# Performance work log

Hardware: AMD Instinct MI355X
Metric: run time of the kernel (lower is better)

The kernel has to match this reference:

```python
import jax, jax.numpy as jnp
import numpy as np

DE_NEIGHBORS = 3
DEPTH = 2


def square_distance(src, dst):
    # src: [B, N, 3], dst: [B, S, 3] -> pairwise squared L2 [B, N, S]
    return (jnp.sum(src * src, axis=-1)[:, :, None]
            + jnp.sum(dst * dst, axis=-1)[:, None, :]
            - 2.0 * jnp.einsum('bnc,bsc->bns', src, dst))


def propagate(xyz1, xyz2, points1, points2):
    # xyz1: [B, N, 3] fine coords; xyz2: [B, S, 3] coarse coords
    # points1: [B, C1, N] skip feats; points2: [B, C2, S] coarse feats
    pts2 = points2.transpose(0, 2, 1)  # [B, S, C2]
    dists = square_distance(xyz1, xyz2)  # [B, N, S]
    neg_d, idx = jax.lax.top_k(-dists, DE_NEIGHBORS)  # smallest-k distances
    d = -neg_d  # [B, N, K]
    w = 1.0 / (d + 1e-8)
    w = w / jnp.sum(w, axis=-1, keepdims=True)  # [B, N, K]
    # gather neighbor features: [B, N, K, C2]
    gathered = jax.vmap(lambda p, i: p[i])(pts2, idx)
    interp = jnp.sum(gathered * w[..., None], axis=2)  # [B, N, C2]
    m = interp.mean()
    s = jnp.std(interp - m, ddof=1)  # torch.std default is unbiased
    interp = (interp - m) / (s + 1e-5)
    new_points = jnp.concatenate([points1.transpose(0, 2, 1), interp], axis=-1)
    return new_points.transpose(0, 2, 1)  # [B, C1+C2, N]


def setup_inputs() -> dict:
    key = jax.random.key(0)
    ks = jax.random.split(key, 6)
    B = 8
    return {
        'xyz0': jax.random.normal(ks[0], (B, 8192, 3), jnp.float32),
        'xyz1': jax.random.normal(ks[1], (B, 2048, 3), jnp.float32),
        'xyz2': jax.random.normal(ks[2], (B, 512, 3), jnp.float32),
        'x0': jax.random.normal(ks[3], (B, 128, 8192), jnp.float32),
        'x1': jax.random.normal(ks[4], (B, 256, 2048), jnp.float32),
        'x2': jax.random.normal(ks[5], (B, 512, 512), jnp.float32),
    }


def reference(xyz0, xyz1, xyz2, x0, x1, x2):
    # forward reverses the lists: index 0 = coarsest level
    xyz_list = [xyz2, xyz1, xyz0]
    x_list = [x2, x1, x0]
    x = x_list[0]
    for i in range(DEPTH):
        x = propagate(xyz_list[i + 1], xyz_list[i], x_list[i + 1], x)
    return x  # [8, 128+256+512, 8192]
```

## Files before the change

kernel.cpp:

```cpp
#include <hip/hip_runtime.h>
#include <cstdint>
#include <math.h>


__device__ __forceinline__ void dev_transpose(const float* __restrict__ in,
                                              float* __restrict__ out,
                                              int C, long in_bs, long out_bs, int out_rs,
                                              int b, int rt, int ct, int tid) {
    __shared__ float tile[32][33];
    const int r0 = rt * 32, c0 = ct * 32;
    const float* inb = in + (size_t)b * in_bs;
    float* outb = out + (size_t)b * out_bs;
    const int tx = tid & 31, ty = tid >> 5;
#pragma unroll
    for (int i = 0; i < 32; i += 8) {
        tile[ty + i][tx] = inb[(size_t)(r0 + ty + i) * C + (c0 + tx)];
    }
    __syncthreads();
#pragma unroll
    for (int i = 0; i < 32; i += 8) {
        outb[(size_t)(c0 + ty + i) * out_rs + (r0 + tx)] = tile[tx][ty + i];
    }
}

__global__ __launch_bounds__(256) void k_setup(const float* __restrict__ xyz1,
                                               const float* __restrict__ xyz2,
                                               const float* __restrict__ x0,
                                               const float* __restrict__ x1,
                                               const float* __restrict__ x2,
                                               float4* __restrict__ c4_2,
                                               float4* __restrict__ c4_1,
                                               float* __restrict__ pts1,
                                               float* __restrict__ inter,
                                               float* __restrict__ out) {
#pragma clang fp contract(off)
    const int id = blockIdx.x;
    const int tid = threadIdx.x;
    if (id < 8192) {
        const size_t i = (size_t)id * 256 + tid;
        const size_t b = i >> 18;
        const size_t off = i & (((size_t)1 << 18) - 1);
        const float4* src = (const float4*)(x0 + b * (size_t)128 * 8192);
        float4* dst = (float4*)(out + b * (size_t)896 * 8192);
        dst[off] = src[off];
    } else if (id < 12288) {
        const int t = id - 8192;
        const int ct = t & 63, rt = (t >> 6) & 7, b = t >> 9;
        dev_transpose(x1, inter, 2048, 256 * 2048, (long)2048 * 768, 768, b, rt, ct, tid);
    } else if (id < 14336) {
        const int t = id - 12288;
        const int ct = t & 15, rt = (t >> 4) & 15, b = t >> 8;
        dev_transpose(x2, pts1, 512, 512 * 512, 512 * 512, 512, b, rt, ct, tid);
    } else {
        const int i = (id - 14336) * 256 + tid;
        const float* src;
        float4* dst;
        if (i < 16384) { src = xyz1 + 3 * (size_t)i; dst = c4_2 + i; }
        else if (i < 20480) { src = xyz2 + 3 * (size_t)(i - 16384); dst = c4_1 + (i - 16384); }
        else return;
        const float x = src[0], y = src[1], z = src[2];
        *dst = make_float4(x, y, z, (x * x + y * y) + z * z);
    }
}

template <int CHUNK>
__device__ __forceinline__ void dev_knn_scan(const float* __restrict__ fine,
                                             const float4* __restrict__ coarse4,
                                             int N, int S, int nch,
                                             int b, int nb, int chunk, int tid,
                                             float* __restrict__ cand_d,
                                             int* __restrict__ cand_i) {
#pragma clang fp contract(off)
    const int n = nb * 256 + tid;
    const int s0 = chunk * CHUNK;
    const float4* cb = coarse4 + (size_t)b * S + s0;
    const float* fp = fine + ((size_t)b * N + n) * 3;
    const float px = fp[0], py = fp[1], pz = fp[2];
    const float psq = (px * px + py * py) + pz * pz;
    float d0 = 1e30f, d1 = 1e30f, d2 = 1e30f;
    int i0 = 0, i1 = 0, i2 = 0;
#pragma unroll 4
    for (int s = 0; s < CHUNK; ++s) {
        const float4 c = cb[s];
        const float dot = (px * c.x + py * c.y) + pz * c.z;
        const float d = fmaf(-2.0f, dot, psq + c.w);
        if (__any(d < d2)) {
            const bool lt0 = d < d0, lt1 = d < d1, lt2 = d < d2;
            d2 = lt1 ? d1 : (lt2 ? d : d2);
            i2 = lt1 ? i1 : (lt2 ? s : i2);
            d1 = lt0 ? d0 : (lt1 ? d : d1);
            i1 = lt0 ? i0 : (lt1 ? s : i1);
            d0 = lt0 ? d : d0;
            i0 = lt0 ? s : i0;
        }
    }
    const size_t p = (((size_t)b * N + n) * nch + chunk) * 3;
    cand_d[p] = d0; cand_d[p + 1] = d1; cand_d[p + 2] = d2;
    cand_i[p] = s0 + i0; cand_i[p + 1] = s0 + i1; cand_i[p + 2] = s0 + i2;
}

__global__ __launch_bounds__(256) void k_knn_all(const float* __restrict__ xyz0,
                                                 const float4* __restrict__ c4_2,
                                                 const float* __restrict__ xyz1,
                                                 const float4* __restrict__ c4_1,
                                                 float* __restrict__ cand_d2,
                                                 int* __restrict__ cand_i2,
                                                 float* __restrict__ cand_d1,
                                                 int* __restrict__ cand_i1) {
    const int id = blockIdx.x;
    const int tid = threadIdx.x;
    if (id < 1024) {
        dev_knn_scan<512>(xyz0, c4_2, 8192, 2048, 4,
                          id >> 7, id & 31, (id >> 5) & 3, tid, cand_d2, cand_i2);
    } else {
        const int t = id - 1024;
        dev_knn_scan<128>(xyz1, c4_1, 2048, 512, 4,
                          t >> 5, t & 7, (t >> 3) & 3, tid, cand_d1, cand_i1);
    }
}

__global__ __launch_bounds__(256) void k_merge(const float* __restrict__ cand_d2,
                                               const int* __restrict__ cand_i2,
                                               const float* __restrict__ cand_d1,
                                               const int* __restrict__ cand_i1,
                                               int* __restrict__ idx2,
                                               float* __restrict__ w2,
                                               int* __restrict__ idx1,
                                               float* __restrict__ w1) {
    int p = blockIdx.x * 256 + threadIdx.x;
    const float* cd; const int* ci; int* idx; float* wout;
    if (p < 65536) { cd = cand_d2; ci = cand_i2; idx = idx2; wout = w2; }
    else { p -= 65536; cd = cand_d1; ci = cand_i1; idx = idx1; wout = w1; }
    cd += (size_t)p * 12; ci += (size_t)p * 12;
    float d0 = 1e30f, d1 = 1e30f, d2 = 1e30f;
    int i0 = 0, i1 = 0, i2 = 0;
#pragma unroll
    for (int k = 0; k < 12; ++k) {
        const float d = cd[k];
        const int s = ci[k];
        const bool lt0 = d < d0, lt1 = d < d1, lt2 = d < d2;
        d2 = lt1 ? d1 : (lt2 ? d : d2);
        i2 = lt1 ? i1 : (lt2 ? s : i2);
        d1 = lt0 ? d0 : (lt1 ? d : d1);
        i1 = lt0 ? i0 : (lt1 ? s : i1);
        d0 = lt0 ? d : d0;
        i0 = lt0 ? s : i0;
    }
    const float w0 = 1.0f / (d0 + 1e-8f);
    const float w1_ = 1.0f / (d1 + 1e-8f);
    const float w2_ = 1.0f / (d2 + 1e-8f);
    const float wsum = (w0 + w1_) + w2_;
    const size_t q = (size_t)p * 3;
    idx[q] = i0; idx[q + 1] = i1; idx[q + 2] = i2;
    wout[q] = w0 / wsum; wout[q + 1] = w1_ / wsum; wout[q + 2] = w2_ / wsum;
}

__global__ __launch_bounds__(256) void k_interp_stats(const float* __restrict__ pts,
                                                      const int* __restrict__ idx,
                                                      const float* __restrict__ w,
                                                      int N, int S, int C,
                                                      double* __restrict__ partials) {
    __shared__ int   si[32][3];
    __shared__ float sw[32][3];
    const int b = blockIdx.x, nb = blockIdx.y, cb = blockIdx.z;
    const int n0 = nb * 32;
    const int tid = threadIdx.x;
    if (tid < 32) {
        size_t p = ((size_t)b * N + n0 + tid) * 3;
        si[tid][0] = idx[p]; si[tid][1] = idx[p + 1]; si[tid][2] = idx[p + 2];
        sw[tid][0] = w[p];   sw[tid][1] = w[p + 1];   sw[tid][2] = w[p + 2];
    }
    __syncthreads();
    const int C4 = C >> 2;
    const float4* pbf = (const float4*)(pts + (size_t)b * S * C) + (cb * 64);
    const int f = tid & 63;
    const int pg = tid >> 6;
    double ls = 0.0, lq = 0.0;
#pragma unroll
    for (int g = 0; g < 8; ++g) {
        const int nl = g * 4 + pg;
        const size_t r0 = (size_t)si[nl][0] * C4;
        const size_t r1 = (size_t)si[nl][1] * C4;
        const size_t r2 = (size_t)si[nl][2] * C4;
        const float w0 = sw[nl][0], w1 = sw[nl][1], w2 = sw[nl][2];
        const float4 a = pbf[r0 + f], c = pbf[r1 + f], e = pbf[r2 + f];
        const float vx = (w0 * a.x + w1 * c.x) + w2 * e.x;
        const float vy = (w0 * a.y + w1 * c.y) + w2 * e.y;
        const float vz = (w0 * a.z + w1 * c.z) + w2 * e.z;
        const float vw = (w0 * a.w + w1 * c.w) + w2 * e.w;
        ls += (double)vx + (double)vy + (double)vz + (double)vw;
        lq += (double)vx * vx + (double)vy * vy + (double)vz * vz + (double)vw * vw;
    }
    __shared__ double sa[256], sb[256];
    sa[tid] = ls; sb[tid] = lq; __syncthreads();
    for (int s = 128; s > 0; s >>= 1) {
        if (tid < s) { sa[tid] += sa[tid + s]; sb[tid] += sb[tid + s]; }
        __syncthreads();
    }
    if (tid == 0) {
        size_t pl = ((size_t)cb * gridDim.x + b) * gridDim.y + nb;
        partials[2 * pl] = sa[0]; partials[2 * pl + 1] = sb[0];
    }
}

__global__ __launch_bounds__(1024) void k_finalize(const double* __restrict__ partials,
                                                   int P, double nelem,
                                                   float* __restrict__ stats) {
    __shared__ double sa[1024], sb[1024];
    double ls = 0.0, lq = 0.0;
    for (int i = threadIdx.x; i < P; i += 1024) { ls += partials[2 * i]; lq += partials[2 * i + 1]; }
    const int t = threadIdx.x;
    sa[t] = ls; sb[t] = lq; __syncthreads();
    for (int s = 512; s > 0; s >>= 1) {
        if (t < s) { sa[t] += sa[t + s]; sb[t] += sb[t + s]; }
        __syncthreads();
    }
    if (t == 0) {
        double sum = sa[0], sq = sb[0];
        double m = sum / nelem;
        double var = (sq - sum * sum / nelem) / (nelem - 1.0);
        double sd = sqrt(var > 0.0 ? var : 0.0);
        stats[0] = (float)m;
        stats[1] = (float)(1.0 / (sd + 1e-5));
    }
}

__global__ __launch_bounds__(256) void k_interp1_write(const float* __restrict__ pts,
                                                       const int* __restrict__ idx,
                                                       const float* __restrict__ w,
                                                       const float* __restrict__ stats,
                                                       float* __restrict__ inter) {
    const float m = stats[0], rs = stats[1];
    const int b = blockIdx.x;
    const int n0 = blockIdx.y * 4;
    const int tid = threadIdx.x;
    const int pt = tid >> 6, f = tid & 63;
    const size_t p = (size_t)b * 2048 + n0 + pt;
    const int i0 = idx[p * 3], i1 = idx[p * 3 + 1], i2 = idx[p * 3 + 2];
    const float w0 = w[p * 3], w1 = w[p * 3 + 1], w2 = w[p * 3 + 2];
    const float4* pb4 = (const float4*)(pts + (size_t)b * 512 * 512);
    const size_t r0 = (size_t)i0 * 128, r1 = (size_t)i1 * 128, r2 = (size_t)i2 * 128;
    float4* out4 = (float4*)(inter + p * 768 + 256);
#pragma unroll
    for (int k = 0; k < 2; ++k) {
        const int c = f + k * 64;
        const float4 a = pb4[r0 + c], d = pb4[r1 + c], e = pb4[r2 + c];
        float4 v;
        v.x = (((w0 * a.x + w1 * d.x) + w2 * e.x) - m) * rs;
        v.y = (((w0 * a.y + w1 * d.y) + w2 * e.y) - m) * rs;
        v.z = (((w0 * a.z + w1 * d.z) + w2 * e.z) - m) * rs;
        v.w = (((w0 * a.w + w1 * d.w) + w2 * e.w) - m) * rs;
        out4[c] = v;
    }
}

__global__ __launch_bounds__(256) void k_interp2_write(const float* __restrict__ pts,
                                                       const int* __restrict__ idx,
                                                       const float* __restrict__ w,
                                                       const float* __restrict__ stats,
                                                       float* __restrict__ out) {
    __shared__ float tile[64][65];
    __shared__ int   si[64][3];
    __shared__ float sw[64][3];
    const float m = stats[0], rs = stats[1];
    const int b = blockIdx.x, nt = blockIdx.y, cc = blockIdx.z;
    const int n0 = nt * 64, c0 = cc * 64;
    const int tid = threadIdx.x;
    if (tid < 64) {
        size_t p = ((size_t)b * 8192 + n0 + tid) * 3;
        si[tid][0] = idx[p]; si[tid][1] = idx[p + 1]; si[tid][2] = idx[p + 2];
        sw[tid][0] = w[p];   sw[tid][1] = w[p + 1];   sw[tid][2] = w[p + 2];
    }
    __syncthreads();
    const float* pb = pts + (size_t)b * 2048 * 768 + c0;
    const int cl = tid & 63;
    const int pg = tid >> 6;
#pragma unroll
    for (int pass = 0; pass < 16; ++pass) {
        const int nl = pass * 4 + pg;
        const float v = (sw[nl][0] * pb[(size_t)si[nl][0] * 768 + cl]
                       + sw[nl][1] * pb[(size_t)si[nl][1] * 768 + cl])
                       + sw[nl][2] * pb[(size_t)si[nl][2] * 768 + cl];
        tile[nl][cl] = (v - m) * rs;
    }
    __syncthreads();
    float* ob = out + (size_t)b * 896 * 8192 + (size_t)(128 + c0) * 8192 + n0;
    const int tn = tid & 63, tc0 = tid >> 6;
#pragma unroll
    for (int pass = 0; pass < 16; ++pass) {
        const int tc = pass * 4 + tc0;
        ob[(size_t)tc * 8192 + tn] = tile[tn][tc];
    }
}

extern "C" void kernel_launch(void* const* d_in, const int* in_sizes, int n_in,
                              void* d_out, int out_size, void* d_ws, size_t ws_size,
                              hipStream_t stream) {
    const float* xyz0 = (const float*)d_in[0];
    const float* xyz1 = (const float*)d_in[1];
    const float* xyz2 = (const float*)d_in[2];
    const float* x0   = (const float*)d_in[3];
    const float* x1   = (const float*)d_in[4];
    const float* x2   = (const float*)d_in[5];
    float* out = (float*)d_out;
    char* ws = (char*)d_ws;

    size_t off = 0;
    auto alloc = [&](size_t bytes) {
        size_t o = off;
        off = (off + bytes + 255) & ~(size_t)255;
        return o;
    };
    float*  stats    = (float*)(ws + alloc(4 * sizeof(float)));
    double* partials = (double*)(ws + alloc((size_t)6144 * 2 * sizeof(double)));
    int*    idx1     = (int*)(ws + alloc((size_t)8 * 2048 * 3 * 4));
    float*  w1       = (float*)(ws + alloc((size_t)8 * 2048 * 3 * 4));
    int*    idx2     = (int*)(ws + alloc((size_t)8 * 8192 * 3 * 4));
    float*  w2       = (float*)(ws + alloc((size_t)8 * 8192 * 3 * 4));
    float4* c4_2     = (float4*)(ws + alloc((size_t)16384 * 16));
    float4* c4_1     = (float4*)(ws + alloc((size_t)4096 * 16));
    float*  pts1     = (float*)(ws + alloc((size_t)8 * 512 * 512 * 4));
    float*  inter    = (float*)(ws + alloc((size_t)8 * 2048 * 768 * 4));
    float*  cand_d2  = (float*)(ws + alloc((size_t)65536 * 12 * 4));
    int*    cand_i2  = (int*)(ws + alloc((size_t)65536 * 12 * 4));
    float*  cand_d1  = (float*)(ws + alloc((size_t)16384 * 12 * 4));
    int*    cand_i1  = (int*)(ws + alloc((size_t)16384 * 12 * 4));

    k_setup<<<14416, 256, 0, stream>>>(xyz1, xyz2, x0, x1, x2,
                                       c4_2, c4_1, pts1, inter, out);
    k_knn_all<<<1280, 256, 0, stream>>>(xyz0, c4_2, xyz1, c4_1,
                                        cand_d2, cand_i2, cand_d1, cand_i1);
    k_merge<<<(65536 + 16384) / 256, 256, 0, stream>>>(cand_d2, cand_i2, cand_d1, cand_i1,
                                                       idx2, w2, idx1, w1);
    k_interp_stats<<<dim3(8, 2048 / 32, 2), 256, 0, stream>>>(
        pts1, idx1, w1, 2048, 512, 512, partials);
    k_finalize<<<1, 1024, 0, stream>>>(partials, 1024, (double)8 * 2048 * 512, stats);
    k_interp1_write<<<dim3(8, 512), 256, 0, stream>>>(pts1, idx1, w1, stats, inter);
    k_interp_stats<<<dim3(8, 8192 / 32, 3), 256, 0, stream>>>(
        inter, idx2, w2, 8192, 2048, 768, partials);
    k_finalize<<<1, 1024, 0, stream>>>(partials, 6144, (double)8 * 8192 * 768, stats + 2);
    k_interp2_write<<<dim3(8, 128, 12), 256, 0, stream>>>(inter, idx2, w2, stats + 2, out);
}
```

Before: 198.5 us.

## Fuse setup and KNN into one front kernel, fold merge and finalize into consumers

```diff
diff --git a/kernel.cpp b/kernel.cpp
--- a/kernel.cpp
+++ b/kernel.cpp
@@ -3,77 +3,49 @@
 #include <math.h>
 
 
-__device__ __forceinline__ void dev_transpose(const float* __restrict__ in,
-                                              float* __restrict__ out,
-                                              int C, long in_bs, long out_bs, int out_rs,
-                                              int b, int rt, int ct, int tid) {
-    __shared__ float tile[32][33];
-    const int r0 = rt * 32, c0 = ct * 32;
-    const float* inb = in + (size_t)b * in_bs;
-    float* outb = out + (size_t)b * out_bs;
-    const int tx = tid & 31, ty = tid >> 5;
-#pragma unroll
-    for (int i = 0; i < 32; i += 8) {
-        tile[ty + i][tx] = inb[(size_t)(r0 + ty + i) * C + (c0 + tx)];
-    }
-    __syncthreads();
-#pragma unroll
-    for (int i = 0; i < 32; i += 8) {
-        outb[(size_t)(c0 + ty + i) * out_rs + (r0 + tx)] = tile[tx][ty + i];
-    }
-}
-
-__global__ __launch_bounds__(256) void k_setup(const float* __restrict__ xyz1,
-                                               const float* __restrict__ xyz2,
-                                               const float* __restrict__ x0,
-                                               const float* __restrict__ x1,
-                                               const float* __restrict__ x2,
-                                               float4* __restrict__ c4_2,
-                                               float4* __restrict__ c4_1,
-                                               float* __restrict__ pts1,
-                                               float* __restrict__ inter,
-                                               float* __restrict__ out) {
+__device__ __forceinline__ void dev_merge6(const float* __restrict__ cd,
+                                           const int* __restrict__ ci,
+                                           int& o0, int& o1, int& o2,
+                                           float& w0, float& w1, float& w2) {
+    float d0 = 1e30f, d1 = 1e30f, d2 = 1e30f;
+    int j0 = 0, j1 = 0, j2 = 0;
+#pragma unroll
+    for (int k = 0; k < 6; ++k) {
+        const float d = cd[k];
+        const int s = ci[k];
+        const bool lt0 = d < d0, lt1 = d < d1, lt2 = d < d2;
+        d2 = lt1 ? d1 : (lt2 ? d : d2);
+        j2 = lt1 ? j1 : (lt2 ? s : j2);
+        d1 = lt0 ? d0 : (lt1 ? d : d1);
+        j1 = lt0 ? j0 : (lt1 ? s : j1);
+        d0 = lt0 ? d : d0;
+        j0 = lt0 ? s : j0;
+    }
+    const float a = 1.0f / (d0 + 1e-8f);
+    const float b = 1.0f / (d1 + 1e-8f);
+    const float c = 1.0f / (d2 + 1e-8f);
+    const float ws = (a + b) + c;
+    o0 = j0; o1 = j1; o2 = j2;
+    w0 = a / ws; w1 = b / ws; w2 = c / ws;
+}
+
+template <int CHUNK>
+__device__ __forceinline__ void dev_knn_lds(const float* __restrict__ fine,
+                                            const float* __restrict__ coarse,
+                                            int N, int S, int nch,
+                                            int b, int nb, int chunk, int tid,
+                                            float4* __restrict__ lc,
+                                            float* __restrict__ cand_d,
+                                            int* __restrict__ cand_i) {
 #pragma clang fp contract(off)
-    const int id = blockIdx.x;
-    const int tid = threadIdx.x;
-    if (id < 8192) {
-        const size_t i = (size_t)id * 256 + tid;
-        const size_t b = i >> 18;
-        const size_t off = i & (((size_t)1 << 18) - 1);
-        const float4* src = (const float4*)(x0 + b * (size_t)128 * 8192);
-        float4* dst = (float4*)(out + b * (size_t)896 * 8192);
-        dst[off] = src[off];
-    } else if (id < 12288) {
-        const int t = id - 8192;
-        const int ct = t & 63, rt = (t >> 6) & 7, b = t >> 9;
-        dev_transpose(x1, inter, 2048, 256 * 2048, (long)2048 * 768, 768, b, rt, ct, tid);
-    } else if (id < 14336) {
-        const int t = id - 12288;
-        const int ct = t & 15, rt = (t >> 4) & 15, b = t >> 8;
-        dev_transpose(x2, pts1, 512, 512 * 512, 512 * 512, 512, b, rt, ct, tid);
-    } else {
-        const int i = (id - 14336) * 256 + tid;
-        const float* src;
-        float4* dst;
-        if (i < 16384) { src = xyz1 + 3 * (size_t)i; dst = c4_2 + i; }
-        else if (i < 20480) { src = xyz2 + 3 * (size_t)(i - 16384); dst = c4_1 + (i - 16384); }
-        else return;
-        const float x = src[0], y = src[1], z = src[2];
-        *dst = make_float4(x, y, z, (x * x + y * y) + z * z);
-    }
-}
-
-template <int CHUNK>
-__device__ __forceinline__ void dev_knn_scan(const float* __restrict__ fine,
-                                             const float4* __restrict__ coarse4,
-                                             int N, int S, int nch,
-                                             int b, int nb, int chunk, int tid,
-                                             float* __restrict__ cand_d,
-                                             int* __restrict__ cand_i) {
-#pragma clang fp contract(off)
+    const int s0 = chunk * CHUNK;
+    const float* cb = coarse + ((size_t)b * S + s0) * 3;
+    for (int s = tid; s < CHUNK; s += 256) {
+        const float x = cb[3 * s], y = cb[3 * s + 1], z = cb[3 * s + 2];
+        lc[s] = make_float4(x, y, z, (x * x + y * y) + z * z);
+    }
+    __syncthreads();
     const int n = nb * 256 + tid;
-    const int s0 = chunk * CHUNK;
-    const float4* cb = coarse4 + (size_t)b * S + s0;
     const float* fp = fine + ((size_t)b * N + n) * 3;
     const float px = fp[0], py = fp[1], pz = fp[2];
     const float psq = (px * px + py * py) + pz * pz;
@@ -81,7 +53,7 @@
     int i0 = 0, i1 = 0, i2 = 0;
 #pragma unroll 4
     for (int s = 0; s < CHUNK; ++s) {
-        const float4 c = cb[s];
+        const float4 c = lc[s];
         const float dot = (px * c.x + py * c.y) + pz * c.z;
         const float d = fmaf(-2.0f, dot, psq + c.w);
         if (__any(d < d2)) {
@@ -99,76 +71,91 @@
     cand_i[p] = s0 + i0; cand_i[p + 1] = s0 + i1; cand_i[p + 2] = s0 + i2;
 }
 
-__global__ __launch_bounds__(256) void k_knn_all(const float* __restrict__ xyz0,
-                                                 const float4* __restrict__ c4_2,
-                                                 const float* __restrict__ xyz1,
-                                                 const float4* __restrict__ c4_1,
-                                                 float* __restrict__ cand_d2,
-                                                 int* __restrict__ cand_i2,
-                                                 float* __restrict__ cand_d1,
-                                                 int* __restrict__ cand_i1) {
+__device__ __forceinline__ void dev_transpose(const float* __restrict__ in,
+                                              float* __restrict__ out,
+                                              int C, long in_bs, long out_bs, int out_rs,
+                                              int b, int rt, int ct, int tid,
+                                              float* __restrict__ tile ) {
+    const int r0 = rt * 32, c0 = ct * 32;
+    const float* inb = in + (size_t)b * in_bs;
+    float* outb = out + (size_t)b * out_bs;
+    const int tx = tid & 31, ty = tid >> 5;
+#pragma unroll
+    for (int i = 0; i < 32; i += 8) {
+        tile[(ty + i) * 33 + tx] = inb[(size_t)(r0 + ty + i) * C + (c0 + tx)];
+    }
+    __syncthreads();
+#pragma unroll
+    for (int i = 0; i < 32; i += 8) {
+        outb[(size_t)(c0 + ty + i) * out_rs + (r0 + tx)] = tile[tx * 33 + (ty + i)];
+    }
+}
+
+__global__ __launch_bounds__(256) void k_front(const float* __restrict__ xyz0,
+                                               const float* __restrict__ xyz1,
+                                               const float* __restrict__ xyz2,
+                                               const float* __restrict__ x0,
+                                               const float* __restrict__ x1,
+                                               const float* __restrict__ x2,
+                                               float* __restrict__ pts1,
+                                               float* __restrict__ inter,
+                                               float* __restrict__ out,
+                                               float* __restrict__ cand_d2,
+                                               int* __restrict__ cand_i2,
+                                               float* __restrict__ cand_d1,
+                                               int* __restrict__ cand_i1,
+                                               unsigned* __restrict__ counters) {
+    __shared__ __align__(16) char smem[16384];
     const int id = blockIdx.x;
     const int tid = threadIdx.x;
-    if (id < 1024) {
-        dev_knn_scan<512>(xyz0, c4_2, 8192, 2048, 4,
-                          id >> 7, id & 31, (id >> 5) & 3, tid, cand_d2, cand_i2);
+    if (id < 512) {
+        dev_knn_lds<1024>(xyz0, xyz1, 8192, 2048, 2,
+                          id >> 6, id & 31, (id >> 5) & 1, tid,
+                          (float4*)smem, cand_d2, cand_i2);
+    } else if (id < 640) {
+        const int t = id - 512;
+        dev_knn_lds<256>(xyz1, xyz2, 2048, 512, 2,
+                         t >> 4, t & 7, (t >> 3) & 1, tid,
+                         (float4*)smem, cand_d1, cand_i1);
+    } else if (id < 8832) {
+        if (id == 640 && tid < 2) counters[tid] = 0;
+        const size_t i = (size_t)(id - 640) * 256 + tid;
+        const size_t b = i >> 18;
+        const size_t off = i & (((size_t)1 << 18) - 1);
+        const float4* src = (const float4*)(x0 + b * (size_t)128 * 8192);
+        float4* dst = (float4*)(out + b * (size_t)896 * 8192);
+        dst[off] = src[off];
+    } else if (id < 12928) {
+        const int t = id - 8832;
+        const int ct = t & 63, rt = (t >> 6) & 7, b = t >> 9;
+        dev_transpose(x1, inter, 2048, 256 * 2048, (long)2048 * 768, 768,
+                      b, rt, ct, tid, (float*)smem);
     } else {
-        const int t = id - 1024;
-        dev_knn_scan<128>(xyz1, c4_1, 2048, 512, 4,
-                          t >> 5, t & 7, (t >> 3) & 3, tid, cand_d1, cand_i1);
-    }
-}
-
-__global__ __launch_bounds__(256) void k_merge(const float* __restrict__ cand_d2,
-                                               const int* __restrict__ cand_i2,
-                                               const float* __restrict__ cand_d1,
-                                               const int* __restrict__ cand_i1,
-                                               int* __restrict__ idx2,
-                                               float* __restrict__ w2,
-                                               int* __restrict__ idx1,
-                                               float* __restrict__ w1) {
-    int p = blockIdx.x * 256 + threadIdx.x;
-    const float* cd; const int* ci; int* idx; float* wout;
-    if (p < 65536) { cd = cand_d2; ci = cand_i2; idx = idx2; wout = w2; }
-    else { p -= 65536; cd = cand_d1; ci = cand_i1; idx = idx1; wout = w1; }
-    cd += (size_t)p * 12; ci += (size_t)p * 12;
-    float d0 = 1e30f, d1 = 1e30f, d2 = 1e30f;
-    int i0 = 0, i1 = 0, i2 = 0;
-#pragma unroll
-    for (int k = 0; k < 12; ++k) {
-        const float d = cd[k];
-        const int s = ci[k];
-        const bool lt0 = d < d0, lt1 = d < d1, lt2 = d < d2;
-        d2 = lt1 ? d1 : (lt2 ? d : d2);
-        i2 = lt1 ? i1 : (lt2 ? s : i2);
-        d1 = lt0 ? d0 : (lt1 ? d : d1);
-        i1 = lt0 ? i0 : (lt1 ? s : i1);
-        d0 = lt0 ? d : d0;
-        i0 = lt0 ? s : i0;
-    }
-    const float w0 = 1.0f / (d0 + 1e-8f);
-    const float w1_ = 1.0f / (d1 + 1e-8f);
-    const float w2_ = 1.0f / (d2 + 1e-8f);
-    const float wsum = (w0 + w1_) + w2_;
-    const size_t q = (size_t)p * 3;
-    idx[q] = i0; idx[q + 1] = i1; idx[q + 2] = i2;
-    wout[q] = w0 / wsum; wout[q + 1] = w1_ / wsum; wout[q + 2] = w2_ / wsum;
+        const int t = id - 12928;
+        const int ct = t & 15, rt = (t >> 4) & 15, b = t >> 8;
+        dev_transpose(x2, pts1, 512, 512 * 512, 512 * 512, 512,
+                      b, rt, ct, tid, (float*)smem);
+    }
 }
 
 __global__ __launch_bounds__(256) void k_interp_stats(const float* __restrict__ pts,
-                                                      const int* __restrict__ idx,
-                                                      const float* __restrict__ w,
+                                                      const float* __restrict__ cand_d,
+                                                      const int* __restrict__ cand_i,
                                                       int N, int S, int C,
-                                                      double* __restrict__ partials) {
+                                                      double* __restrict__ partials,
+                                                      float* __restrict__ stats_out,
+                                                      unsigned* __restrict__ counter,
+                                                      int nblocks, double nelem) {
     __shared__ int   si[32][3];
     __shared__ float sw[32][3];
     const int b = blockIdx.x, nb = blockIdx.y, cb = blockIdx.z;
     const int n0 = nb * 32;
     const int tid = threadIdx.x;
     if (tid < 32) {
-        size_t p = ((size_t)b * N + n0 + tid) * 3;
-        si[tid][0] = idx[p]; si[tid][1] = idx[p + 1]; si[tid][2] = idx[p + 2];
-        sw[tid][0] = w[p];   sw[tid][1] = w[p + 1];   sw[tid][2] = w[p + 2];
+        const size_t pt = (size_t)b * N + n0 + tid;
+        dev_merge6(cand_d + pt * 6, cand_i + pt * 6,
+                   si[tid][0], si[tid][1], si[tid][2],
+                   sw[tid][0], sw[tid][1], sw[tid][2]);
     }
     __syncthreads();
     const int C4 = C >> 2;
@@ -197,37 +184,38 @@
         if (tid < s) { sa[tid] += sa[tid + s]; sb[tid] += sb[tid + s]; }
         __syncthreads();
     }
+    __shared__ unsigned ticket;
     if (tid == 0) {
-        size_t pl = ((size_t)cb * gridDim.x + b) * gridDim.y + nb;
+        const size_t pl = ((size_t)cb * gridDim.x + b) * gridDim.y + nb;
         partials[2 * pl] = sa[0]; partials[2 * pl + 1] = sb[0];
-    }
-}
-
-__global__ __launch_bounds__(1024) void k_finalize(const double* __restrict__ partials,
-                                                   int P, double nelem,
-                                                   float* __restrict__ stats) {
-    __shared__ double sa[1024], sb[1024];
-    double ls = 0.0, lq = 0.0;
-    for (int i = threadIdx.x; i < P; i += 1024) { ls += partials[2 * i]; lq += partials[2 * i + 1]; }
-    const int t = threadIdx.x;
-    sa[t] = ls; sb[t] = lq; __syncthreads();
-    for (int s = 512; s > 0; s >>= 1) {
-        if (t < s) { sa[t] += sa[t + s]; sb[t] += sb[t + s]; }
-        __syncthreads();
-    }
-    if (t == 0) {
-        double sum = sa[0], sq = sb[0];
-        double m = sum / nelem;
-        double var = (sq - sum * sum / nelem) / (nelem - 1.0);
-        double sd = sqrt(var > 0.0 ? var : 0.0);
-        stats[0] = (float)m;
-        stats[1] = (float)(1.0 / (sd + 1e-5));
+        __threadfence();
+        ticket = atomicAdd(counter, 1u);
+    }
+    __syncthreads();
+    if (ticket == (unsigned)(nblocks - 1)) {
+        __threadfence();
+        double fs = 0.0, fq = 0.0;
+        for (int i = tid; i < nblocks; i += 256) { fs += partials[2 * i]; fq += partials[2 * i + 1]; }
+        sa[tid] = fs; sb[tid] = fq; __syncthreads();
+        for (int s = 128; s > 0; s >>= 1) {
+            if (tid < s) { sa[tid] += sa[tid + s]; sb[tid] += sb[tid + s]; }
+            __syncthreads();
+        }
+        if (tid == 0) {
+            const double sum = sa[0], sq = sb[0];
+            const double m = sum / nelem;
+            const double var = (sq - sum * sum / nelem) / (nelem - 1.0);
+            const double sd = sqrt(var > 0.0 ? var : 0.0);
+            stats_out[0] = (float)m;
+            stats_out[1] = (float)(1.0 / (sd + 1e-5));
+            *counter = 0;
+        }
     }
 }
 
 __global__ __launch_bounds__(256) void k_interp1_write(const float* __restrict__ pts,
-                                                       const int* __restrict__ idx,
-                                                       const float* __restrict__ w,
+                                                       const float* __restrict__ cand_d,
+                                                       const int* __restrict__ cand_i,
                                                        const float* __restrict__ stats,
                                                        float* __restrict__ inter) {
     const float m = stats[0], rs = stats[1];
@@ -236,8 +224,8 @@
     const int tid = threadIdx.x;
     const int pt = tid >> 6, f = tid & 63;
     const size_t p = (size_t)b * 2048 + n0 + pt;
-    const int i0 = idx[p * 3], i1 = idx[p * 3 + 1], i2 = idx[p * 3 + 2];
-    const float w0 = w[p * 3], w1 = w[p * 3 + 1], w2 = w[p * 3 + 2];
+    int i0, i1, i2; float w0, w1, w2;
+    dev_merge6(cand_d + p * 6, cand_i + p * 6, i0, i1, i2, w0, w1, w2);
     const float4* pb4 = (const float4*)(pts + (size_t)b * 512 * 512);
     const size_t r0 = (size_t)i0 * 128, r1 = (size_t)i1 * 128, r2 = (size_t)i2 * 128;
     float4* out4 = (float4*)(inter + p * 768 + 256);
@@ -255,8 +243,8 @@
 }
 
 __global__ __launch_bounds__(256) void k_interp2_write(const float* __restrict__ pts,
-                                                       const int* __restrict__ idx,
-                                                       const float* __restrict__ w,
+                                                       const float* __restrict__ cand_d,
+                                                       const int* __restrict__ cand_i,
                                                        const float* __restrict__ stats,
                                                        float* __restrict__ out) {
     __shared__ float tile[64][65];
@@ -267,9 +255,10 @@
     const int n0 = nt * 64, c0 = cc * 64;
     const int tid = threadIdx.x;
     if (tid < 64) {
-        size_t p = ((size_t)b * 8192 + n0 + tid) * 3;
-        si[tid][0] = idx[p]; si[tid][1] = idx[p + 1]; si[tid][2] = idx[p + 2];
-        sw[tid][0] = w[p];   sw[tid][1] = w[p + 1];   sw[tid][2] = w[p + 2];
+        const size_t pt = (size_t)b * 8192 + n0 + tid;
+        dev_merge6(cand_d + pt * 6, cand_i + pt * 6,
+                   si[tid][0], si[tid][1], si[tid][2],
+                   sw[tid][0], sw[tid][1], sw[tid][2]);
     }
     __syncthreads();
     const float* pb = pts + (size_t)b * 2048 * 768 + c0;
@@ -311,33 +300,26 @@
         off = (off + bytes + 255) & ~(size_t)255;
         return o;
     };
-    float*  stats    = (float*)(ws + alloc(4 * sizeof(float)));
-    double* partials = (double*)(ws + alloc((size_t)6144 * 2 * sizeof(double)));
-    int*    idx1     = (int*)(ws + alloc((size_t)8 * 2048 * 3 * 4));
-    float*  w1       = (float*)(ws + alloc((size_t)8 * 2048 * 3 * 4));
-    int*    idx2     = (int*)(ws + alloc((size_t)8 * 8192 * 3 * 4));
-    float*  w2       = (float*)(ws + alloc((size_t)8 * 8192 * 3 * 4));
-    float4* c4_2     = (float4*)(ws + alloc((size_t)16384 * 16));
-    float4* c4_1     = (float4*)(ws + alloc((size_t)4096 * 16));
-    float*  pts1     = (float*)(ws + alloc((size_t)8 * 512 * 512 * 4));
-    float*  inter    = (float*)(ws + alloc((size_t)8 * 2048 * 768 * 4));
-    float*  cand_d2  = (float*)(ws + alloc((size_t)65536 * 12 * 4));
-    int*    cand_i2  = (int*)(ws + alloc((size_t)65536 * 12 * 4));
-    float*  cand_d1  = (float*)(ws + alloc((size_t)16384 * 12 * 4));
-    int*    cand_i1  = (int*)(ws + alloc((size_t)16384 * 12 * 4));
-
-    k_setup<<<14416, 256, 0, stream>>>(xyz1, xyz2, x0, x1, x2,
-                                       c4_2, c4_1, pts1, inter, out);
-    k_knn_all<<<1280, 256, 0, stream>>>(xyz0, c4_2, xyz1, c4_1,
-                                        cand_d2, cand_i2, cand_d1, cand_i1);
-    k_merge<<<(65536 + 16384) / 256, 256, 0, stream>>>(cand_d2, cand_i2, cand_d1, cand_i1,
-                                                       idx2, w2, idx1, w1);
-    k_interp_stats<<<dim3(8, 2048 / 32, 2), 256, 0, stream>>>(
-        pts1, idx1, w1, 2048, 512, 512, partials);
-    k_finalize<<<1, 1024, 0, stream>>>(partials, 1024, (double)8 * 2048 * 512, stats);
-    k_interp1_write<<<dim3(8, 512), 256, 0, stream>>>(pts1, idx1, w1, stats, inter);
-    k_interp_stats<<<dim3(8, 8192 / 32, 3), 256, 0, stream>>>(
-        inter, idx2, w2, 8192, 2048, 768, partials);
-    k_finalize<<<1, 1024, 0, stream>>>(partials, 6144, (double)8 * 8192 * 768, stats + 2);
-    k_interp2_write<<<dim3(8, 128, 12), 256, 0, stream>>>(inter, idx2, w2, stats + 2, out);
-}
+    float*    stats    = (float*)(ws + alloc(8 * sizeof(float)));
+    unsigned* counters = (unsigned*)(ws + alloc(8 * sizeof(unsigned)));
+    double*   partials = (double*)(ws + alloc((size_t)6144 * 2 * sizeof(double)));
+    float*    pts1     = (float*)(ws + alloc((size_t)8 * 512 * 512 * 4));
+    float*    inter    = (float*)(ws + alloc((size_t)8 * 2048 * 768 * 4));
+    float*    cand_d2  = (float*)(ws + alloc((size_t)65536 * 6 * 4));
+    int*      cand_i2  = (int*)(ws + alloc((size_t)65536 * 6 * 4));
+    float*    cand_d1  = (float*)(ws + alloc((size_t)16384 * 6 * 4));
+    int*      cand_i1  = (int*)(ws + alloc((size_t)16384 * 6 * 4));
+
+    k_front<<<14976, 256, 0, stream>>>(xyz0, xyz1, xyz2, x0, x1, x2,
+                                       pts1, inter, out,
+                                       cand_d2, cand_i2, cand_d1, cand_i1, counters);
+    k_interp_stats<<<dim3(8, 64, 2), 256, 0, stream>>>(
+        pts1, cand_d1, cand_i1, 2048, 512, 512, partials,
+        stats, counters, 1024, (double)8 * 2048 * 512);
+    k_interp1_write<<<dim3(8, 512), 256, 0, stream>>>(pts1, cand_d1, cand_i1, stats, inter);
+    k_interp_stats<<<dim3(8, 256, 3), 256, 0, stream>>>(
+        inter, cand_d2, cand_i2, 8192, 2048, 768, partials,
+        stats + 2, counters + 1, 6144, (double)8 * 8192 * 768);
+    k_interp2_write<<<dim3(8, 128, 12), 256, 0, stream>>>(inter, cand_d2, cand_i2,
+                                                          stats + 2, out);
+}
```

Result: slower. 364.3 us (+83.5%).
